# Kernel tuning notes

Measured on AMD Instinct MI355X. Metric: run time of the kernel, lower is better.

## Reference

```python
import jax, jax.numpy as jnp
import numpy as np

B, S, D = 2, 2048, 1024
H = 16
DK = D // H  # 64


def _rope_tables():
    # standard RoPE frequencies, shaped (1,1,S,DK//2) for clean broadcasting
    half = DK // 2
    inv_freq = 1.0 / (10000.0 ** (np.arange(0, half, dtype=np.float32) * 2.0 / DK))
    t = np.arange(S, dtype=np.float32)
    ang = np.einsum('s,d->sd', t, inv_freq)  # (S, half)
    sin = jnp.asarray(np.sin(ang))[None, None]  # (1,1,S,half)
    cos = jnp.asarray(np.cos(ang))[None, None]
    return sin, cos


def setup_inputs() -> dict:
    key = jax.random.key(0)
    ks = jax.random.split(key, 12)
    scale = 1.0 / np.sqrt(D)
    k = jax.random.normal(ks[0], (B, S, D), jnp.float32)
    q = jax.random.normal(ks[1], (B, S, D), jnp.float32)
    v = jax.random.normal(ks[2], (B, S, D), jnp.float32)
    # causal mask, broadcast over batch and heads: (1,1,S,S)
    mask = jnp.tril(jnp.ones((S, S), jnp.int32))[None, None]
    sin, cos = _rope_tables()
    Wk = jax.random.normal(ks[3], (D, D), jnp.float32) * scale
    bk = jax.random.normal(ks[4], (D,), jnp.float32) * scale
    Wq = jax.random.normal(ks[5], (D, D), jnp.float32) * scale
    bq = jax.random.normal(ks[6], (D,), jnp.float32) * scale
    Wv = jax.random.normal(ks[7], (D, D), jnp.float32) * scale
    bv = jax.random.normal(ks[8], (D,), jnp.float32) * scale
    Wo = jax.random.normal(ks[9], (D, D), jnp.float32) * scale
    bo = jax.random.normal(ks[10], (D,), jnp.float32) * scale
    return dict(k=k, q=q, v=v, mask=mask, sin=sin, cos=cos,
                Wk=Wk, bk=bk, Wq=Wq, bq=bq, Wv=Wv, bv=bv, Wo=Wo, bo=bo)


def _apply_rope(x, sin, cos):
    # x: (B,H,S,DK); sin/cos: (1,1,S,DK//2)
    x1 = x[..., ::2]
    x2 = x[..., 1::2]
    even = x1 * cos - x2 * sin
    odd = x1 * sin + x2 * cos
    return jnp.stack((even, odd), axis=-1).reshape(x.shape)


def reference(k, q, v, mask, sin, cos, Wk, bk, Wq, bq, Wv, bv, Wo, bo):
    # projections (nn.Linear: x @ W.T + b)
    def proj(x, W, b):
        y = x @ W.T + b
        return y.reshape(B, S, H, DK).transpose(0, 2, 1, 3)  # (B,H,S,DK)

    key = proj(k, Wk, bk)
    query = proj(q, Wq, bq)
    value = proj(v, Wv, bv)

    query = _apply_rope(query, sin, cos)
    key = _apply_rope(key, sin, cos)

    scores = jnp.einsum('bhqd,bhkd->bhqk', query, key) / jnp.sqrt(jnp.float32(DK))
    scores = jnp.where(mask == 0, jnp.float32(-1e9), scores)
    attn = jax.nn.softmax(scores, axis=-1)  # dropout=0 -> identity
    x = jnp.einsum('bhqk,bhkd->bhqd', attn, value)
    x = x.transpose(0, 2, 1, 3).reshape(B, S, D)
    return x @ Wo.T + bo
```

## Files before the change

kernel.cpp:

```cpp
#include <hip/hip_runtime.h>
#include <hip/hip_bf16.h>

typedef __bf16 bf16x8 __attribute__((ext_vector_type(8)));
typedef __bf16 bf16x4 __attribute__((ext_vector_type(4)));
typedef float  f32x4  __attribute__((ext_vector_type(4)));

static constexpr int B = 2, S = 2048, D = 1024, H = 16, DK = 64;
static constexpr int M = B * S;
static constexpr int NE = M * D;
static constexpr int WE = D * D;

__device__ inline float fast_exp2(float x) { return __builtin_amdgcn_exp2f(x); }

__device__ inline void gload16(const void* g, void* l) {
  __builtin_amdgcn_global_load_lds(
      (const __attribute__((address_space(1))) void*)g,
      (__attribute__((address_space(3))) void*)l, 16, 0, 0);
}

__device__ inline int perm64(int i) {
  return (((i >> 2) & 3) << 4) | (((i >> 5) & 1) << 3) | (((i >> 4) & 1) << 2) | (i & 3);
}

__global__ __launch_bounds__(256) void cvt_w(
    const float* __restrict__ Wq, const float* __restrict__ Wk,
    const float* __restrict__ Wv, const float* __restrict__ Wo,
    __bf16* __restrict__ Wall)
{
  int z = blockIdx.y;
  const float* src = (z == 0) ? Wq : (z == 1) ? Wk : (z == 2) ? Wv : Wo;
  __bf16* dst = Wall + (size_t)z * WE;
  int n4 = WE / 4;
  int i = blockIdx.x * blockDim.x + threadIdx.x;
  int stride = gridDim.x * blockDim.x;
  for (; i < n4; i += stride) {
    float4 f = reinterpret_cast<const float4*>(src)[i];
    bf16x4 o;
    o[0] = (__bf16)f.x; o[1] = (__bf16)f.y; o[2] = (__bf16)f.z; o[3] = (__bf16)f.w;
    reinterpret_cast<bf16x4*>(dst)[i] = o;
  }
}

__global__ __launch_bounds__(256, 4) void proj_kernel(
    const float* __restrict__ Xq32, const float* __restrict__ Xk32,
    const float* __restrict__ Xv32, const __bf16* __restrict__ Wall,
    const float* __restrict__ bq_, const float* __restrict__ bk_,
    const float* __restrict__ bv_,
    const float* __restrict__ sinp, const float* __restrict__ cosp,
    __bf16* __restrict__ Qr, __bf16* __restrict__ Kr, __bf16* __restrict__ Vt)
{
  __shared__ __align__(16) __bf16 Ws[128 * 64];
  __shared__ __align__(16) __bf16 Xs[128 * 64];
  int tid = threadIdx.x;
  int lane = tid & 63, wid = tid >> 6;
  int lr = lane & 15, lg = lane >> 4;
  int wr = wid >> 1, wc = wid & 1;
  int m0 = blockIdx.x * 128;
  int by = blockIdx.y;
  int z  = by >> 3;
  const float*  X32  = (z == 0) ? Xq32 : (z == 1) ? Xk32 : Xv32;
  const __bf16* Bw   = Wall + (size_t)by * 128 * 1024;
  const float*  bias = (z == 0) ? bq_ : (z == 1) ? bk_ : bv_;

  int wrow = tid >> 3;
  int wcol = 8 * ((tid & 7) ^ ((tid >> 3) & 7));
  char* wsbase = (char*)Ws + wid * 1024;

  int xrow = tid >> 3;
  int xcolf = (tid & 7) * 8;
  int xwb = ((tid & 7) * 16) ^ (((tid >> 3) & 7) << 4);

  f32x4 acc[4][4];
#pragma unroll
  for (int i = 0; i < 4; ++i)
#pragma unroll
    for (int j = 0; j < 4; ++j) acc[i][j] = (f32x4){0, 0, 0, 0};

  int fsw = (lr & 7) << 4;
  int foff0 = (lg * 16) ^ fsw;
  int foff1 = (64 + lg * 16) ^ fsw;

  bf16x8 xb[4];
#pragma unroll
  for (int p = 0; p < 4; ++p) {
    const float* xp = X32 + (size_t)(m0 + p * 32 + xrow) * 1024 + xcolf;
    f32x4 a = *(const f32x4*)(xp);
    f32x4 b = *(const f32x4*)(xp + 4);
    bf16x8 v;
#pragma unroll
    for (int e = 0; e < 4; ++e) { v[e] = (__bf16)a[e]; v[4 + e] = (__bf16)b[e]; }
    xb[p] = v;
  }

  for (int k0 = 0; k0 < 1024; k0 += 64) {
#pragma unroll
    for (int c = 0; c < 4; ++c)
      gload16(Bw + (size_t)(c * 32 + wrow) * 1024 + k0 + wcol,
              wsbase + c * 4096);
#pragma unroll
    for (int p = 0; p < 4; ++p)
      *(bf16x8*)((char*)Xs + (p * 32 + xrow) * 128 + xwb) = xb[p];
    __syncthreads();
    if (k0 + 64 < 1024) {
#pragma unroll
      for (int p = 0; p < 4; ++p) {
        const float* xp = X32 + (size_t)(m0 + p * 32 + xrow) * 1024 + k0 + 64 + xcolf;
        f32x4 a = *(const f32x4*)(xp);
        f32x4 b = *(const f32x4*)(xp + 4);
        bf16x8 v;
#pragma unroll
        for (int e = 0; e < 4; ++e) { v[e] = (__bf16)a[e]; v[4 + e] = (__bf16)b[e]; }
        xb[p] = v;
      }
    }
#pragma unroll
    for (int h = 0; h < 2; ++h) {
      int fo = h ? foff1 : foff0;
      bf16x8 af[4], bfr[4];
#pragma unroll
      for (int mi = 0; mi < 4; ++mi)
        af[mi] = *(const bf16x8*)((char*)Ws + (wr * 64 + mi * 16 + lr) * 128 + fo);
#pragma unroll
      for (int ni = 0; ni < 4; ++ni)
        bfr[ni] = *(const bf16x8*)((char*)Xs + (wc * 64 + ni * 16 + lr) * 128 + fo);
#pragma unroll
      for (int mi = 0; mi < 4; ++mi)
#pragma unroll
        for (int ni = 0; ni < 4; ++ni)
          acc[mi][ni] = __builtin_amdgcn_mfma_f32_16x16x32_bf16(af[mi], bfr[ni], acc[mi][ni], 0, 0, 0);
    }
    __syncthreads();
  }

#pragma unroll
  for (int mi = 0; mi < 4; ++mi) {
    int dkf0 = by * 128 + wr * 64 + mi * 16 + lg * 4;
    int col0 = dkf0 & 1023;
    int h = col0 >> 6, dk0 = col0 & 63, t0 = dk0 >> 1;
    float4 bv4 = *reinterpret_cast<const float4*>(&bias[col0]);
#pragma unroll
    for (int ni = 0; ni < 4; ++ni) {
      int r = m0 + wc * 64 + ni * 16 + lr;
      int s = r & (S - 1), bb = r >> 11;
      float v0 = acc[mi][ni][0] + bv4.x;
      float v1 = acc[mi][ni][1] + bv4.y;
      float v2 = acc[mi][ni][2] + bv4.z;
      float v3 = acc[mi][ni][3] + bv4.w;
      if (z < 2) {
        float2 sn = *reinterpret_cast<const float2*>(&sinp[s * 32 + t0]);
        float2 cs = *reinterpret_cast<const float2*>(&cosp[s * 32 + t0]);
        float e0 = v0 * cs.x - v1 * sn.x, o0 = v0 * sn.x + v1 * cs.x;
        float e1 = v2 * cs.y - v3 * sn.y, o1 = v2 * sn.y + v3 * cs.y;
        if (z == 0) {
          e0 *= 0.18033688011112042f; o0 *= 0.18033688011112042f;
          e1 *= 0.18033688011112042f; o1 *= 0.18033688011112042f;
        }
        bf16x4 w;
        w[0] = (__bf16)e0; w[1] = (__bf16)o0; w[2] = (__bf16)e1; w[3] = (__bf16)o1;
        __bf16* dst = (z == 0) ? Qr : Kr;
        *(bf16x4*)&dst[((size_t)(bb * H + h) * S + s) * DK + dk0] = w;
      } else {
        int sp = (s & ~63) | perm64(s & 63);
        size_t base = ((size_t)(bb * H + h) * DK + dk0) * S + sp;
        Vt[base]         = (__bf16)v0;
        Vt[base + S]     = (__bf16)v1;
        Vt[base + 2 * S] = (__bf16)v2;
        Vt[base + 3 * S] = (__bf16)v3;
      }
    }
  }
}

__global__ __launch_bounds__(256) void outproj_kernel(
    const __bf16* __restrict__ AO, const __bf16* __restrict__ Wo,
    const float* __restrict__ bo_, float* __restrict__ out)
{
  __shared__ __align__(16) __bf16 As[64 * 32];
  __shared__ __align__(16) __bf16 Bs[128 * 32];
  int tid = threadIdx.x;
  int lane = tid & 63, wid = tid >> 6;
  int lr = lane & 15, lg = lane >> 4;
  int wr = wid >> 1, wc = wid & 1;
  int m0 = blockIdx.x * 64;
  int n0 = blockIdx.y * 128;

  int arow = tid >> 2;
  int acol = (tid & 3) * 8;
  int brow = tid >> 2;
  int bcol = (tid & 3) * 8;
  char* asw = (char*)As + wid * 1024;
  char* bsw = (char*)Bs + wid * 1024;

  f32x4 acc[4][2];
#pragma unroll
  for (int i = 0; i < 4; ++i)
#pragma unroll
    for (int j = 0; j < 2; ++j) acc[i][j] = (f32x4){0, 0, 0, 0};

  for (int k0 = 0; k0 < 1024; k0 += 32) {
    gload16(AO + (size_t)(m0 + arow) * 1024 + k0 + acol, asw);
    gload16(Wo + (size_t)(n0 + brow) * 1024 + k0 + bcol, bsw);
    gload16(Wo + (size_t)(n0 + brow + 64) * 1024 + k0 + bcol, bsw + 4096);
    __syncthreads();
    bf16x8 wf[4], aof[2];
#pragma unroll
    for (int mi = 0; mi < 4; ++mi)
      wf[mi]  = *reinterpret_cast<const bf16x8*>(&Bs[(wr*64 + mi*16 + lr)*32 + lg*8]);
#pragma unroll
    for (int ni = 0; ni < 2; ++ni)
      aof[ni] = *reinterpret_cast<const bf16x8*>(&As[(wc*32 + ni*16 + lr)*32 + lg*8]);
#pragma unroll
    for (int mi = 0; mi < 4; ++mi)
#pragma unroll
      for (int ni = 0; ni < 2; ++ni)
        acc[mi][ni] = __builtin_amdgcn_mfma_f32_16x16x32_bf16(wf[mi], aof[ni], acc[mi][ni], 0, 0, 0);
    __syncthreads();
  }

#pragma unroll
  for (int mi = 0; mi < 4; ++mi) {
    int c0 = n0 + wr * 64 + mi * 16 + lg * 4;
    float4 bv4 = *reinterpret_cast<const float4*>(&bo_[c0]);
#pragma unroll
    for (int ni = 0; ni < 2; ++ni) {
      int r = m0 + wc * 32 + ni * 16 + lr;
      float4 w;
      w.x = acc[mi][ni][0] + bv4.x;
      w.y = acc[mi][ni][1] + bv4.y;
      w.z = acc[mi][ni][2] + bv4.z;
      w.w = acc[mi][ni][3] + bv4.w;
      *reinterpret_cast<float4*>(&out[(size_t)r * 1024 + c0]) = w;
    }
  }
}

__global__ __launch_bounds__(256, 4) void attn_kernel(
    const __bf16* __restrict__ Qr, const __bf16* __restrict__ Kr,
    const __bf16* __restrict__ Vt, __bf16* __restrict__ AO)
{
  __shared__ __align__(16) char smem[32768];
  int tid = threadIdx.x;
  int lane = tid & 63, wid = tid >> 6;
  int lr = lane & 15, lg = lane >> 4;
  int bx = blockIdx.x;
  int bh = (bx & 7) * 4 + ((bx >> 3) & 3);
  int qb = 31 - (bx >> 5);
  int q0 = qb * 64 + wid * 16;
  int nsteps = qb + 1;

  const char* Kb = (const char*)(Kr + (size_t)bh * S * DK);
  const char* Vb = (const char*)(Vt + (size_t)bh * DK * S);
  const __bf16* Qh = Qr + (size_t)bh * S * DK;

  int o_lo = wid * 1024 + lane * 16;
#define STAGE(sel, kv0)                                                        \
  {                                                                            \
    char* kdst = smem + (sel) * 16384;                                         \
    _Pragma("unroll")                                                          \
    for (int i = 0; i < 2; ++i) {                                              \
      int o = o_lo + i * 4096;                                                 \
      int row = o >> 7;                                                        \
      int colp = (o & 127) ^ ((row & 7) << 4);                                 \
      gload16(Kb + (((size_t)((kv0) + row)) << 7) + colp,                      \
              kdst + wid * 1024 + i * 4096);                                   \
      gload16(Vb + ((size_t)row * S + (kv0)) * 2 + colp,                       \
              kdst + 8192 + wid * 1024 + i * 4096);                            \
    }                                                                          \
  }

  bf16x8 bq[2];
#pragma unroll
  for (int kc = 0; kc < 2; ++kc)
    bq[kc] = *(const bf16x8*)(Qh + (size_t)(q0 + lr) * DK + kc * 32 + lg * 8);

  int swz = (lr & 7) << 4;
  int oK0 = lr * 128 + ((lg * 16) ^ swz);
  int oK1 = lr * 128 + ((64 + lg * 16) ^ swz);
  int oV0 = lr * 128 + ((lg * 32) ^ swz);
  int oV1 = lr * 128 + ((16 + lg * 32) ^ swz);

  f32x4 o[4];
  float m2 = -3e38f, l2 = 0.f;
#pragma unroll
  for (int dt = 0; dt < 4; ++dt) o[dt] = (f32x4){0, 0, 0, 0};

  STAGE(0, 0);
  __syncthreads();

  for (int j = 0; j < nsteps; ++j) {
    int sel = j & 1;
    if (j + 1 < nsteps) STAGE(sel ^ 1, (j + 1) * 64);
    const char* kbuf = smem + sel * 16384;
    const char* vbuf = kbuf + 8192;
    int kv0 = j * 64;

    f32x4 sc[4];
#pragma unroll
    for (int kt = 0; kt < 4; ++kt) {
      bf16x8 ka0 = *(const bf16x8*)(kbuf + oK0 + kt * 2048);
      bf16x8 ka1 = *(const bf16x8*)(kbuf + oK1 + kt * 2048);
      f32x4 s = (f32x4){0, 0, 0, 0};
      s = __builtin_amdgcn_mfma_f32_16x16x32_bf16(ka0, bq[0], s, 0, 0, 0);
      s = __builtin_amdgcn_mfma_f32_16x16x32_bf16(ka1, bq[1], s, 0, 0, 0);
      sc[kt] = s;
    }

    if (j == qb) {
#pragma unroll
      for (int kt = 0; kt < 4; ++kt)
#pragma unroll
        for (int i = 0; i < 4; ++i)
          if (kv0 + kt * 16 + lg * 4 + i > q0 + lr)
            sc[kt][i] = -3e38f;
    }

    float tm = fmaxf(
        fmaxf(fmaxf(fmaxf(sc[0][0], sc[0][1]), fmaxf(sc[0][2], sc[0][3])),
              fmaxf(fmaxf(sc[1][0], sc[1][1]), fmaxf(sc[1][2], sc[1][3]))),
        fmaxf(fmaxf(fmaxf(sc[2][0], sc[2][1]), fmaxf(sc[2][2], sc[2][3])),
              fmaxf(fmaxf(sc[3][0], sc[3][1]), fmaxf(sc[3][2], sc[3][3]))));
    tm = fmaxf(tm, __shfl_xor(tm, 16));
    tm = fmaxf(tm, __shfl_xor(tm, 32));
    if (__any(tm > m2 + 8.0f)) {
      float mn = fmaxf(m2, tm);
      float f = fast_exp2(m2 - mn);
      m2 = mn;
      l2 *= f;
#pragma unroll
      for (int dt = 0; dt < 4; ++dt) o[dt] *= f;
    }
    float p[16];
#pragma unroll
    for (int kt = 0; kt < 4; ++kt)
#pragma unroll
      for (int i = 0; i < 4; ++i)
        p[kt * 4 + i] = fast_exp2(sc[kt][i] - m2);
    float sum = (((p[0] + p[1]) + (p[2] + p[3])) + ((p[4] + p[5]) + (p[6] + p[7]))) +
                (((p[8] + p[9]) + (p[10] + p[11])) + ((p[12] + p[13]) + (p[14] + p[15])));
    sum += __shfl_xor(sum, 16);
    sum += __shfl_xor(sum, 32);
    l2 += sum;
    bf16x8 pb[2];
#pragma unroll
    for (int kc = 0; kc < 2; ++kc) {
      bf16x8 pv;
#pragma unroll
      for (int a = 0; a < 2; ++a)
#pragma unroll
        for (int r = 0; r < 4; ++r)
          pv[a * 4 + r] = (__bf16)p[(2 * kc + a) * 4 + r];
      pb[kc] = pv;
    }

#pragma unroll
    for (int dt = 0; dt < 4; ++dt) {
      bf16x8 v0 = *(const bf16x8*)(vbuf + oV0 + dt * 2048);
      bf16x8 v1 = *(const bf16x8*)(vbuf + oV1 + dt * 2048);
      o[dt] = __builtin_amdgcn_mfma_f32_16x16x32_bf16(v0, pb[0], o[dt], 0, 0, 0);
      o[dt] = __builtin_amdgcn_mfma_f32_16x16x32_bf16(v1, pb[1], o[dt], 0, 0, 0);
    }
    __syncthreads();
  }
#undef STAGE

  int b = bh >> 4, h = bh & 15;
  float inv = 1.f / l2;
  int s = q0 + lr;
#pragma unroll
  for (int dt = 0; dt < 4; ++dt) {
    bf16x4 w;
#pragma unroll
    for (int i = 0; i < 4; ++i) w[i] = (__bf16)(o[dt][i] * inv);
    *(bf16x4*)&AO[(((size_t)(b * S + s)) * H + h) * DK + dt * 16 + lg * 4] = w;
  }
}

extern "C" void kernel_launch(void* const* d_in, const int* in_sizes, int n_in,
                              void* d_out, int out_size, void* d_ws, size_t ws_size,
                              hipStream_t stream) {
  const float* k_in = (const float*)d_in[0];
  const float* q_in = (const float*)d_in[1];
  const float* v_in = (const float*)d_in[2];
  const float* sinp = (const float*)d_in[4];
  const float* cosp = (const float*)d_in[5];
  const float* Wk = (const float*)d_in[6];
  const float* bk = (const float*)d_in[7];
  const float* Wq = (const float*)d_in[8];
  const float* bq = (const float*)d_in[9];
  const float* Wv = (const float*)d_in[10];
  const float* bv = (const float*)d_in[11];
  const float* Wo = (const float*)d_in[12];
  const float* bo = (const float*)d_in[13];
  float* out = (float*)d_out;

  __bf16* ws   = (__bf16*)d_ws;
  __bf16* Wall = ws;
  __bf16* Qr   = ws + 4 * WE;
  __bf16* Kr   = Qr + NE;
  __bf16* Vt   = Kr + NE;
  __bf16* AO   = Vt + NE;

  dim3 blk(256);
  cvt_w<<<dim3(512, 4), blk, 0, stream>>>(Wq, Wk, Wv, Wo, Wall);
  proj_kernel<<<dim3(32, 24), blk, 0, stream>>>(q_in, k_in, v_in, Wall, bq, bk, bv,
                                                sinp, cosp, Qr, Kr, Vt);
  attn_kernel<<<1024, blk, 0, stream>>>(Qr, Kr, Vt, AO);
  outproj_kernel<<<dim3(64, 8), blk, 0, stream>>>(AO, Wall + 3 * WE, bo, out);
}
```

Before: 107.6 us.

## Double-buffer weight tiles in projection and out-projection GEMMs

Both GEMM kernels now keep two LDS buffers for the global-to-LDS weight (and activation) tiles and issue the next tile's async loads before the current tile's MFMAs. The goal is to overlap global load latency with compute and to cut one full __syncthreads per iteration. The projection kernel also holds raw fp32 X prefetches in registers and converts them just before the LDS store, and uses a bare s_barrier at the end of each iteration. The cost is double the LDS footprint and more live registers, which may lower occupancy. Correctness depends on the async LDS loads being complete before they are read, with only an s_barrier and no explicit vmcnt wait in between.

After: 127.7 us. 1.19x slower.

```diff
diff --git a/kernel.cpp b/kernel.cpp
--- a/kernel.cpp
+++ b/kernel.cpp
@@ -16,6 +16,12 @@
   __builtin_amdgcn_global_load_lds(
       (const __attribute__((address_space(1))) void*)g,
       (__attribute__((address_space(3))) void*)l, 16, 0, 0);
+}
+
+__device__ inline void bare_barrier() {
+  asm volatile("" ::: "memory");
+  __builtin_amdgcn_s_barrier();
+  asm volatile("" ::: "memory");
 }
 
 __device__ inline int perm64(int i) {
@@ -49,7 +55,7 @@
     const float* __restrict__ sinp, const float* __restrict__ cosp,
     __bf16* __restrict__ Qr, __bf16* __restrict__ Kr, __bf16* __restrict__ Vt)
 {
-  __shared__ __align__(16) __bf16 Ws[128 * 64];
+  __shared__ __align__(16) __bf16 Ws[2 * 128 * 64];
   __shared__ __align__(16) __bf16 Xs[128 * 64];
   int tid = threadIdx.x;
   int lane = tid & 63, wid = tid >> 6;
@@ -64,11 +70,10 @@
 
   int wrow = tid >> 3;
   int wcol = 8 * ((tid & 7) ^ ((tid >> 3) & 7));
-  char* wsbase = (char*)Ws + wid * 1024;
-
   int xrow = tid >> 3;
   int xcolf = (tid & 7) * 8;
   int xwb = ((tid & 7) * 16) ^ (((tid >> 3) & 7) << 4);
+  const float* xbase = X32 + (size_t)(m0 + xrow) * 1024 + xcolf;
 
   f32x4 acc[4][4];
 #pragma unroll
@@ -80,46 +85,52 @@
   int foff0 = (lg * 16) ^ fsw;
   int foff1 = (64 + lg * 16) ^ fsw;
 
-  bf16x8 xb[4];
+  f32x4 xf[8];
 #pragma unroll
   for (int p = 0; p < 4; ++p) {
-    const float* xp = X32 + (size_t)(m0 + p * 32 + xrow) * 1024 + xcolf;
-    f32x4 a = *(const f32x4*)(xp);
-    f32x4 b = *(const f32x4*)(xp + 4);
-    bf16x8 v;
-#pragma unroll
-    for (int e = 0; e < 4; ++e) { v[e] = (__bf16)a[e]; v[4 + e] = (__bf16)b[e]; }
-    xb[p] = v;
-  }
-
-  for (int k0 = 0; k0 < 1024; k0 += 64) {
+    xf[2*p]   = *(const f32x4*)(xbase + p * 32 * 1024);
+    xf[2*p+1] = *(const f32x4*)(xbase + p * 32 * 1024 + 4);
+  }
+  {
+    char* wd = (char*)Ws + wid * 1024;
 #pragma unroll
     for (int c = 0; c < 4; ++c)
-      gload16(Bw + (size_t)(c * 32 + wrow) * 1024 + k0 + wcol,
-              wsbase + c * 4096);
-#pragma unroll
-    for (int p = 0; p < 4; ++p)
-      *(bf16x8*)((char*)Xs + (p * 32 + xrow) * 128 + xwb) = xb[p];
+      gload16(Bw + (size_t)(c * 32 + wrow) * 1024 + wcol, wd + c * 4096);
+  }
+
+#pragma clang loop unroll(disable)
+  for (int t = 0; t < 16; ++t) {
+    int k0 = t * 64;
+    int kn = (t < 15) ? k0 + 64 : k0;
+#pragma unroll
+    for (int p = 0; p < 4; ++p) {
+      bf16x8 v;
+#pragma unroll
+      for (int e = 0; e < 4; ++e) {
+        v[e] = (__bf16)xf[2*p][e]; v[4+e] = (__bf16)xf[2*p+1][e];
+      }
+      *(bf16x8*)((char*)Xs + (p * 32 + xrow) * 128 + xwb) = v;
+    }
     __syncthreads();
-    if (k0 + 64 < 1024) {
-#pragma unroll
-      for (int p = 0; p < 4; ++p) {
-        const float* xp = X32 + (size_t)(m0 + p * 32 + xrow) * 1024 + k0 + 64 + xcolf;
-        f32x4 a = *(const f32x4*)(xp);
-        f32x4 b = *(const f32x4*)(xp + 4);
-        bf16x8 v;
-#pragma unroll
-        for (int e = 0; e < 4; ++e) { v[e] = (__bf16)a[e]; v[4 + e] = (__bf16)b[e]; }
-        xb[p] = v;
-      }
-    }
+#pragma unroll
+    for (int p = 0; p < 4; ++p) {
+      xf[2*p]   = *(const f32x4*)(xbase + p * 32 * 1024 + kn);
+      xf[2*p+1] = *(const f32x4*)(xbase + p * 32 * 1024 + kn + 4);
+    }
+    {
+      char* wd = (char*)Ws + (((t + 1) & 1) << 14) + wid * 1024;
+#pragma unroll
+      for (int c = 0; c < 4; ++c)
+        gload16(Bw + (size_t)(c * 32 + wrow) * 1024 + kn + wcol, wd + c * 4096);
+    }
+    const char* wsr = (const char*)Ws + ((t & 1) << 14);
 #pragma unroll
     for (int h = 0; h < 2; ++h) {
       int fo = h ? foff1 : foff0;
       bf16x8 af[4], bfr[4];
 #pragma unroll
       for (int mi = 0; mi < 4; ++mi)
-        af[mi] = *(const bf16x8*)((char*)Ws + (wr * 64 + mi * 16 + lr) * 128 + fo);
+        af[mi] = *(const bf16x8*)(wsr + (wr * 64 + mi * 16 + lr) * 128 + fo);
 #pragma unroll
       for (int ni = 0; ni < 4; ++ni)
         bfr[ni] = *(const bf16x8*)((char*)Xs + (wc * 64 + ni * 16 + lr) * 128 + fo);
@@ -129,7 +140,7 @@
         for (int ni = 0; ni < 4; ++ni)
           acc[mi][ni] = __builtin_amdgcn_mfma_f32_16x16x32_bf16(af[mi], bfr[ni], acc[mi][ni], 0, 0, 0);
     }
-    __syncthreads();
+    bare_barrier();
   }
 
 #pragma unroll
@@ -175,8 +186,8 @@
     const __bf16* __restrict__ AO, const __bf16* __restrict__ Wo,
     const float* __restrict__ bo_, float* __restrict__ out)
 {
-  __shared__ __align__(16) __bf16 As[64 * 32];
-  __shared__ __align__(16) __bf16 Bs[128 * 32];
+  __shared__ __align__(16) __bf16 As[2 * 64 * 32];
+  __shared__ __align__(16) __bf16 Bs[2 * 128 * 32];
   int tid = threadIdx.x;
   int lane = tid & 63, wid = tid >> 6;
   int lr = lane & 15, lg = lane >> 4;
@@ -186,10 +197,6 @@
 
   int arow = tid >> 2;
   int acol = (tid & 3) * 8;
-  int brow = tid >> 2;
-  int bcol = (tid & 3) * 8;
-  char* asw = (char*)As + wid * 1024;
-  char* bsw = (char*)Bs + wid * 1024;
 
   f32x4 acc[4][2];
 #pragma unroll
@@ -197,24 +204,39 @@
 #pragma unroll
     for (int j = 0; j < 2; ++j) acc[i][j] = (f32x4){0, 0, 0, 0};
 
-  for (int k0 = 0; k0 < 1024; k0 += 32) {
-    gload16(AO + (size_t)(m0 + arow) * 1024 + k0 + acol, asw);
-    gload16(Wo + (size_t)(n0 + brow) * 1024 + k0 + bcol, bsw);
-    gload16(Wo + (size_t)(n0 + brow + 64) * 1024 + k0 + bcol, bsw + 4096);
+  {
+    char* asw = (char*)As + wid * 1024;
+    char* bsw = (char*)Bs + wid * 1024;
+    gload16(AO + (size_t)(m0 + arow) * 1024 + acol, asw);
+    gload16(Wo + (size_t)(n0 + arow) * 1024 + acol, bsw);
+    gload16(Wo + (size_t)(n0 + arow + 64) * 1024 + acol, bsw + 4096);
+  }
+
+#pragma clang loop unroll(disable)
+  for (int t = 0; t < 32; ++t) {
+    int kn = (t < 31) ? (t + 1) * 32 : t * 32;
     __syncthreads();
+    {
+      char* asw = (char*)As + (((t + 1) & 1) << 12) + wid * 1024;
+      char* bsw = (char*)Bs + (((t + 1) & 1) << 13) + wid * 1024;
+      gload16(AO + (size_t)(m0 + arow) * 1024 + kn + acol, asw);
+      gload16(Wo + (size_t)(n0 + arow) * 1024 + kn + acol, bsw);
+      gload16(Wo + (size_t)(n0 + arow + 64) * 1024 + kn + acol, bsw + 4096);
+    }
+    const __bf16* as = (const __bf16*)((const char*)As + ((t & 1) << 12));
+    const __bf16* bs = (const __bf16*)((const char*)Bs + ((t & 1) << 13));
     bf16x8 wf[4], aof[2];
 #pragma unroll
     for (int mi = 0; mi < 4; ++mi)
-      wf[mi]  = *reinterpret_cast<const bf16x8*>(&Bs[(wr*64 + mi*16 + lr)*32 + lg*8]);
+      wf[mi]  = *reinterpret_cast<const bf16x8*>(&bs[(wr*64 + mi*16 + lr)*32 + lg*8]);
 #pragma unroll
     for (int ni = 0; ni < 2; ++ni)
-      aof[ni] = *reinterpret_cast<const bf16x8*>(&As[(wc*32 + ni*16 + lr)*32 + lg*8]);
+      aof[ni] = *reinterpret_cast<const bf16x8*>(&as[(wc*32 + ni*16 + lr)*32 + lg*8]);
 #pragma unroll
     for (int mi = 0; mi < 4; ++mi)
 #pragma unroll
       for (int ni = 0; ni < 2; ++ni)
         acc[mi][ni] = __builtin_amdgcn_mfma_f32_16x16x32_bf16(wf[mi], aof[ni], acc[mi][ni], 0, 0, 0);
-    __syncthreads();
   }
 
 #pragma unroll
```

## Coalesce projection epilogue stores via LDS staging and transposed V MFMA

Applied to the files above, without the earlier changes.

The Q/K epilogue now stages rotated bf16 results in shared memory with an XOR swizzle and writes them out as 16-byte row-contiguous stores instead of scattered 8-byte ones. For V, the MFMA operands are swapped so each lane holds four consecutive sequence positions, letting the transposed Vt be written with bf16x4 vector stores rather than four scalar strided stores. The X prefetch now keeps fp32 values in registers and converts at LDS-store time, which raises register pressure. This adds a barrier and extra LDS traffic in the epilogue.

Result: slower. 375.6 us (+249.0%).

```diff
diff --git a/kernel.cpp b/kernel.cpp
--- a/kernel.cpp
+++ b/kernel.cpp
@@ -49,8 +49,9 @@
     const float* __restrict__ sinp, const float* __restrict__ cosp,
     __bf16* __restrict__ Qr, __bf16* __restrict__ Kr, __bf16* __restrict__ Vt)
 {
-  __shared__ __align__(16) __bf16 Ws[128 * 64];
-  __shared__ __align__(16) __bf16 Xs[128 * 64];
+  __shared__ __align__(16) char psm[32768];
+  char* Wsc = psm;
+  char* Xsc = psm + 16384;
   int tid = threadIdx.x;
   int lane = tid & 63, wid = tid >> 6;
   int lr = lane & 15, lg = lane >> 4;
@@ -64,11 +65,12 @@
 
   int wrow = tid >> 3;
   int wcol = 8 * ((tid & 7) ^ ((tid >> 3) & 7));
-  char* wsbase = (char*)Ws + wid * 1024;
+  char* wsbase = Wsc + wid * 1024;
 
   int xrow = tid >> 3;
   int xcolf = (tid & 7) * 8;
   int xwb = ((tid & 7) * 16) ^ (((tid >> 3) & 7) << 4);
+  const float* xbase = X32 + (size_t)(m0 + xrow) * 1024 + xcolf;
 
   f32x4 acc[4][4];
 #pragma unroll
@@ -80,38 +82,44 @@
   int foff0 = (lg * 16) ^ fsw;
   int foff1 = (64 + lg * 16) ^ fsw;
 
-  bf16x8 xb[4];
-#pragma unroll
-  for (int p = 0; p < 4; ++p) {
-    const float* xp = X32 + (size_t)(m0 + p * 32 + xrow) * 1024 + xcolf;
-    f32x4 a = *(const f32x4*)(xp);
-    f32x4 b = *(const f32x4*)(xp + 4);
-    bf16x8 v;
-#pragma unroll
-    for (int e = 0; e < 4; ++e) { v[e] = (__bf16)a[e]; v[4 + e] = (__bf16)b[e]; }
-    xb[p] = v;
-  }
+  f32x4 xa0 = *(const f32x4*)(xbase);
+  f32x4 xa1 = *(const f32x4*)(xbase + 4);
+  f32x4 xa2 = *(const f32x4*)(xbase + 32 * 1024);
+  f32x4 xa3 = *(const f32x4*)(xbase + 32 * 1024 + 4);
+  f32x4 xa4 = *(const f32x4*)(xbase + 64 * 1024);
+  f32x4 xa5 = *(const f32x4*)(xbase + 64 * 1024 + 4);
+  f32x4 xa6 = *(const f32x4*)(xbase + 96 * 1024);
+  f32x4 xa7 = *(const f32x4*)(xbase + 96 * 1024 + 4);
 
   for (int k0 = 0; k0 < 1024; k0 += 64) {
 #pragma unroll
     for (int c = 0; c < 4; ++c)
-      gload16(Bw + (size_t)(c * 32 + wrow) * 1024 + k0 + wcol,
-              wsbase + c * 4096);
-#pragma unroll
-    for (int p = 0; p < 4; ++p)
-      *(bf16x8*)((char*)Xs + (p * 32 + xrow) * 128 + xwb) = xb[p];
+      gload16(Bw + (size_t)(c * 32 + wrow) * 1024 + k0 + wcol, wsbase + c * 4096);
+    {
+      bf16x8 v0, v1, v2, v3;
+#pragma unroll
+      for (int e = 0; e < 4; ++e) {
+        v0[e] = (__bf16)xa0[e]; v0[4+e] = (__bf16)xa1[e];
+        v1[e] = (__bf16)xa2[e]; v1[4+e] = (__bf16)xa3[e];
+        v2[e] = (__bf16)xa4[e]; v2[4+e] = (__bf16)xa5[e];
+        v3[e] = (__bf16)xa6[e]; v3[4+e] = (__bf16)xa7[e];
+      }
+      *(bf16x8*)(Xsc + (0 * 32 + xrow) * 128 + xwb) = v0;
+      *(bf16x8*)(Xsc + (1 * 32 + xrow) * 128 + xwb) = v1;
+      *(bf16x8*)(Xsc + (2 * 32 + xrow) * 128 + xwb) = v2;
+      *(bf16x8*)(Xsc + (3 * 32 + xrow) * 128 + xwb) = v3;
+    }
     __syncthreads();
     if (k0 + 64 < 1024) {
-#pragma unroll
-      for (int p = 0; p < 4; ++p) {
-        const float* xp = X32 + (size_t)(m0 + p * 32 + xrow) * 1024 + k0 + 64 + xcolf;
-        f32x4 a = *(const f32x4*)(xp);
-        f32x4 b = *(const f32x4*)(xp + 4);
-        bf16x8 v;
-#pragma unroll
-        for (int e = 0; e < 4; ++e) { v[e] = (__bf16)a[e]; v[4 + e] = (__bf16)b[e]; }
-        xb[p] = v;
-      }
+      const float* xn = xbase + k0 + 64;
+      xa0 = *(const f32x4*)(xn);
+      xa1 = *(const f32x4*)(xn + 4);
+      xa2 = *(const f32x4*)(xn + 32 * 1024);
+      xa3 = *(const f32x4*)(xn + 32 * 1024 + 4);
+      xa4 = *(const f32x4*)(xn + 64 * 1024);
+      xa5 = *(const f32x4*)(xn + 64 * 1024 + 4);
+      xa6 = *(const f32x4*)(xn + 96 * 1024);
+      xa7 = *(const f32x4*)(xn + 96 * 1024 + 4);
     }
 #pragma unroll
     for (int h = 0; h < 2; ++h) {
@@ -119,34 +127,43 @@
       bf16x8 af[4], bfr[4];
 #pragma unroll
       for (int mi = 0; mi < 4; ++mi)
-        af[mi] = *(const bf16x8*)((char*)Ws + (wr * 64 + mi * 16 + lr) * 128 + fo);
+        af[mi] = *(const bf16x8*)(Wsc + (wr * 64 + mi * 16 + lr) * 128 + fo);
 #pragma unroll
       for (int ni = 0; ni < 4; ++ni)
-        bfr[ni] = *(const bf16x8*)((char*)Xs + (wc * 64 + ni * 16 + lr) * 128 + fo);
-#pragma unroll
-      for (int mi = 0; mi < 4; ++mi)
-#pragma unroll
-        for (int ni = 0; ni < 4; ++ni)
-          acc[mi][ni] = __builtin_amdgcn_mfma_f32_16x16x32_bf16(af[mi], bfr[ni], acc[mi][ni], 0, 0, 0);
-    }
-    __syncthreads();
-  }
-
-#pragma unroll
-  for (int mi = 0; mi < 4; ++mi) {
-    int dkf0 = by * 128 + wr * 64 + mi * 16 + lg * 4;
-    int col0 = dkf0 & 1023;
-    int h = col0 >> 6, dk0 = col0 & 63, t0 = dk0 >> 1;
-    float4 bv4 = *reinterpret_cast<const float4*>(&bias[col0]);
-#pragma unroll
-    for (int ni = 0; ni < 4; ++ni) {
-      int r = m0 + wc * 64 + ni * 16 + lr;
-      int s = r & (S - 1), bb = r >> 11;
-      float v0 = acc[mi][ni][0] + bv4.x;
-      float v1 = acc[mi][ni][1] + bv4.y;
-      float v2 = acc[mi][ni][2] + bv4.z;
-      float v3 = acc[mi][ni][3] + bv4.w;
+        bfr[ni] = *(const bf16x8*)(Xsc + (wc * 64 + ni * 16 + lr) * 128 + fo);
       if (z < 2) {
+#pragma unroll
+        for (int mi = 0; mi < 4; ++mi)
+#pragma unroll
+          for (int ni = 0; ni < 4; ++ni)
+            acc[mi][ni] = __builtin_amdgcn_mfma_f32_16x16x32_bf16(af[mi], bfr[ni], acc[mi][ni], 0, 0, 0);
+      } else {
+#pragma unroll
+        for (int mi = 0; mi < 4; ++mi)
+#pragma unroll
+          for (int ni = 0; ni < 4; ++ni)
+            acc[mi][ni] = __builtin_amdgcn_mfma_f32_16x16x32_bf16(bfr[ni], af[mi], acc[mi][ni], 0, 0, 0);
+      }
+    }
+    __syncthreads();
+  }
+
+  if (z < 2) {
+    char* L = psm;
+#pragma unroll
+    for (int mi = 0; mi < 4; ++mi) {
+      int dkb = wr * 64 + mi * 16 + lg * 4;
+      int col0 = (by * 128 + dkb) & 1023;
+      int t0 = (col0 & 63) >> 1;
+      float4 bv4 = *reinterpret_cast<const float4*>(&bias[col0]);
+#pragma unroll
+      for (int ni = 0; ni < 4; ++ni) {
+        int srow = wc * 64 + ni * 16 + lr;
+        int s = (m0 + srow) & (S - 1);
+        float v0 = acc[mi][ni][0] + bv4.x;
+        float v1 = acc[mi][ni][1] + bv4.y;
+        float v2 = acc[mi][ni][2] + bv4.z;
+        float v3 = acc[mi][ni][3] + bv4.w;
         float2 sn = *reinterpret_cast<const float2*>(&sinp[s * 32 + t0]);
         float2 cs = *reinterpret_cast<const float2*>(&cosp[s * 32 + t0]);
         float e0 = v0 * cs.x - v1 * sn.x, o0 = v0 * sn.x + v1 * cs.x;
@@ -157,15 +174,37 @@
         }
         bf16x4 w;
         w[0] = (__bf16)e0; w[1] = (__bf16)o0; w[2] = (__bf16)e1; w[3] = (__bf16)o1;
-        __bf16* dst = (z == 0) ? Qr : Kr;
-        *(bf16x4*)&dst[((size_t)(bb * H + h) * S + s) * DK + dk0] = w;
-      } else {
-        int sp = (s & ~63) | perm64(s & 63);
-        size_t base = ((size_t)(bb * H + h) * DK + dk0) * S + sp;
-        Vt[base]         = (__bf16)v0;
-        Vt[base + S]     = (__bf16)v1;
-        Vt[base + 2 * S] = (__bf16)v2;
-        Vt[base + 3 * S] = (__bf16)v3;
+        *(bf16x4*)(L + srow * 256 + ((dkb * 2) ^ ((srow & 7) << 4))) = w;
+      }
+    }
+    __syncthreads();
+    __bf16* dst = (z == 0) ? Qr : Kr;
+#pragma unroll
+    for (int it = 0; it < 8; ++it) {
+      int srow = (tid >> 4) + 16 * it;
+      int c = tid & 15;
+      bf16x8 v = *(const bf16x8*)(psm + srow * 256 + ((c * 16) ^ ((srow & 7) << 4)));
+      int r = m0 + srow;
+      int s = r & (S - 1), bb = r >> 11;
+      int col0 = (by * 128 + c * 8) & 1023;
+      int h = col0 >> 6, dk0 = col0 & 63;
+      *(bf16x8*)&dst[((size_t)(bb * H + h) * S + s) * DK + dk0] = v;
+    }
+  } else {
+#pragma unroll
+    for (int mi = 0; mi < 4; ++mi) {
+      int col0 = (by * 128 + wr * 64 + mi * 16 + lr) & 1023;
+      int h = col0 >> 6, dk = col0 & 63;
+      float bval = bias[col0];
+#pragma unroll
+      for (int ni = 0; ni < 4; ++ni) {
+        int s0 = m0 + wc * 64 + ni * 16 + lg * 4;
+        int sg = s0 & (S - 1), bb = s0 >> 11;
+        int sp = (sg & ~63) | perm64(sg & 63);
+        bf16x4 w;
+#pragma unroll
+        for (int i = 0; i < 4; ++i) w[i] = (__bf16)(acc[mi][ni][i] + bval);
+        *(bf16x4*)&Vt[((size_t)(bb * H + h) * DK + dk) * S + sp] = w;
       }
     }
   }
@@ -186,8 +225,6 @@
 
   int arow = tid >> 2;
   int acol = (tid & 3) * 8;
-  int brow = tid >> 2;
-  int bcol = (tid & 3) * 8;
   char* asw = (char*)As + wid * 1024;
   char* bsw = (char*)Bs + wid * 1024;
 
@@ -199,8 +236,8 @@
 
   for (int k0 = 0; k0 < 1024; k0 += 32) {
     gload16(AO + (size_t)(m0 + arow) * 1024 + k0 + acol, asw);
-    gload16(Wo + (size_t)(n0 + brow) * 1024 + k0 + bcol, bsw);
-    gload16(Wo + (size_t)(n0 + brow + 64) * 1024 + k0 + bcol, bsw + 4096);
+    gload16(Wo + (size_t)(n0 + arow) * 1024 + k0 + acol, bsw);
+    gload16(Wo + (size_t)(n0 + arow + 64) * 1024 + k0 + acol, bsw + 4096);
     __syncthreads();
     bf16x8 wf[4], aof[2];
 #pragma unroll
```

## Double-buffer projection GEMM LDS tiles with K=32 steps and two-deep prefetch

Applied to the files above, without the earlier changes.

Restructures the QKV projection main loop to use two shared-memory buffers with a 32-wide K step. The next tile's weights (async global-to-LDS) and converted activations are written into the other buffer while MFMAs run on the current one, and fp32 activations are loaded two steps ahead. This removes the second barrier per iteration and is meant to hide load latency, at the cost of more iterations, doubled shared memory and a new swizzle scheme. The output projection change is only a variable rename.

New measurement: 114.9 us. 1.07x slower.

```diff
diff --git a/kernel.cpp b/kernel.cpp
--- a/kernel.cpp
+++ b/kernel.cpp
@@ -49,8 +49,7 @@
     const float* __restrict__ sinp, const float* __restrict__ cosp,
     __bf16* __restrict__ Qr, __bf16* __restrict__ Kr, __bf16* __restrict__ Vt)
 {
-  __shared__ __align__(16) __bf16 Ws[128 * 64];
-  __shared__ __align__(16) __bf16 Xs[128 * 64];
+  __shared__ __align__(16) char smem[32768];
   int tid = threadIdx.x;
   int lane = tid & 63, wid = tid >> 6;
   int lr = lane & 15, lg = lane >> 4;
@@ -62,13 +61,16 @@
   const __bf16* Bw   = Wall + (size_t)by * 128 * 1024;
   const float*  bias = (z == 0) ? bq_ : (z == 1) ? bk_ : bv_;
 
-  int wrow = tid >> 3;
-  int wcol = 8 * ((tid & 7) ^ ((tid >> 3) & 7));
-  char* wsbase = (char*)Ws + wid * 1024;
-
-  int xrow = tid >> 3;
-  int xcolf = (tid & 7) * 8;
-  int xwb = ((tid & 7) * 16) ^ (((tid >> 3) & 7) << 4);
+  int wrb   = wid * 16 + (lane >> 2);
+  int wcolE = ((lane & 3) * 8) ^ (((lane >> 2) & 3) << 3);
+
+  int xr = tid >> 1, xc = tid & 1;
+  const float* xbase = X32 + (size_t)(m0 + xr) * 1024 + xc * 16;
+  int xswz = (xr & 3) << 4;
+  int xo0 = xr * 64 + ((xc * 32) ^ xswz);
+  int xo1 = xr * 64 + ((xc * 32 + 16) ^ xswz);
+
+  int foff = (lg * 16) ^ ((lr & 3) << 4);
 
   f32x4 acc[4][4];
 #pragma unroll
@@ -76,53 +78,62 @@
 #pragma unroll
     for (int j = 0; j < 4; ++j) acc[i][j] = (f32x4){0, 0, 0, 0};
 
-  int fsw = (lr & 7) << 4;
-  int foff0 = (lg * 16) ^ fsw;
-  int foff1 = (64 + lg * 16) ^ fsw;
-
-  bf16x8 xb[4];
-#pragma unroll
-  for (int p = 0; p < 4; ++p) {
-    const float* xp = X32 + (size_t)(m0 + p * 32 + xrow) * 1024 + xcolf;
-    f32x4 a = *(const f32x4*)(xp);
-    f32x4 b = *(const f32x4*)(xp + 4);
-    bf16x8 v;
-#pragma unroll
-    for (int e = 0; e < 4; ++e) { v[e] = (__bf16)a[e]; v[4 + e] = (__bf16)b[e]; }
-    xb[p] = v;
-  }
-
-  for (int k0 = 0; k0 < 1024; k0 += 64) {
-#pragma unroll
-    for (int c = 0; c < 4; ++c)
-      gload16(Bw + (size_t)(c * 32 + wrow) * 1024 + k0 + wcol,
-              wsbase + c * 4096);
-#pragma unroll
-    for (int p = 0; p < 4; ++p)
-      *(bf16x8*)((char*)Xs + (p * 32 + xrow) * 128 + xwb) = xb[p];
-    __syncthreads();
-    if (k0 + 64 < 1024) {
-#pragma unroll
-      for (int p = 0; p < 4; ++p) {
-        const float* xp = X32 + (size_t)(m0 + p * 32 + xrow) * 1024 + k0 + 64 + xcolf;
-        f32x4 a = *(const f32x4*)(xp);
-        f32x4 b = *(const f32x4*)(xp + 4);
-        bf16x8 v;
-#pragma unroll
-        for (int e = 0; e < 4; ++e) { v[e] = (__bf16)a[e]; v[4 + e] = (__bf16)b[e]; }
-        xb[p] = v;
+  f32x4 xa0 = *(const f32x4*)(xbase);
+  f32x4 xa1 = *(const f32x4*)(xbase + 4);
+  f32x4 xa2 = *(const f32x4*)(xbase + 8);
+  f32x4 xa3 = *(const f32x4*)(xbase + 12);
+  {
+    bf16x8 lo, hi;
+#pragma unroll
+    for (int e = 0; e < 4; ++e) {
+      lo[e] = (__bf16)xa0[e]; lo[4 + e] = (__bf16)xa1[e];
+      hi[e] = (__bf16)xa2[e]; hi[4 + e] = (__bf16)xa3[e];
+    }
+    *(bf16x8*)(smem + 8192 + xo0) = lo;
+    *(bf16x8*)(smem + 8192 + xo1) = hi;
+    char* wd = smem + wid * 1024;
+    gload16(Bw + (size_t)wrb * 1024 + wcolE, wd);
+    gload16(Bw + (size_t)(64 + wrb) * 1024 + wcolE, wd + 4096);
+  }
+  xa0 = *(const f32x4*)(xbase + 32);
+  xa1 = *(const f32x4*)(xbase + 36);
+  xa2 = *(const f32x4*)(xbase + 40);
+  xa3 = *(const f32x4*)(xbase + 44);
+  __syncthreads();
+
+#pragma clang loop unroll(disable)
+  for (int t = 0; t < 32; ++t) {
+    int cur = t & 1, nxt = cur ^ 1;
+    char* bufC = smem + cur * 16384;
+    char* bufN = smem + nxt * 16384;
+    int kn  = (t < 31) ? (t + 1) * 32 : 31 * 32;
+    int kn2 = (t < 30) ? (t + 2) * 32 : 31 * 32;
+
+    {
+      char* wd = bufN + wid * 1024;
+      gload16(Bw + (size_t)wrb * 1024 + kn + wcolE, wd);
+      gload16(Bw + (size_t)(64 + wrb) * 1024 + kn + wcolE, wd + 4096);
+      bf16x8 lo, hi;
+#pragma unroll
+      for (int e = 0; e < 4; ++e) {
+        lo[e] = (__bf16)xa0[e]; lo[4 + e] = (__bf16)xa1[e];
+        hi[e] = (__bf16)xa2[e]; hi[4 + e] = (__bf16)xa3[e];
       }
-    }
-#pragma unroll
-    for (int h = 0; h < 2; ++h) {
-      int fo = h ? foff1 : foff0;
+      *(bf16x8*)(bufN + 8192 + xo0) = lo;
+      *(bf16x8*)(bufN + 8192 + xo1) = hi;
+    }
+    xa0 = *(const f32x4*)(xbase + kn2);
+    xa1 = *(const f32x4*)(xbase + kn2 + 4);
+    xa2 = *(const f32x4*)(xbase + kn2 + 8);
+    xa3 = *(const f32x4*)(xbase + kn2 + 12);
+    {
       bf16x8 af[4], bfr[4];
 #pragma unroll
       for (int mi = 0; mi < 4; ++mi)
-        af[mi] = *(const bf16x8*)((char*)Ws + (wr * 64 + mi * 16 + lr) * 128 + fo);
+        af[mi] = *(const bf16x8*)(bufC + (wr * 64 + mi * 16 + lr) * 64 + foff);
 #pragma unroll
       for (int ni = 0; ni < 4; ++ni)
-        bfr[ni] = *(const bf16x8*)((char*)Xs + (wc * 64 + ni * 16 + lr) * 128 + fo);
+        bfr[ni] = *(const bf16x8*)(bufC + 8192 + (wc * 64 + ni * 16 + lr) * 64 + foff);
 #pragma unroll
       for (int mi = 0; mi < 4; ++mi)
 #pragma unroll
@@ -186,8 +197,6 @@
 
   int arow = tid >> 2;
   int acol = (tid & 3) * 8;
-  int brow = tid >> 2;
-  int bcol = (tid & 3) * 8;
   char* asw = (char*)As + wid * 1024;
   char* bsw = (char*)Bs + wid * 1024;
 
@@ -199,8 +208,8 @@
 
   for (int k0 = 0; k0 < 1024; k0 += 32) {
     gload16(AO + (size_t)(m0 + arow) * 1024 + k0 + acol, asw);
-    gload16(Wo + (size_t)(n0 + brow) * 1024 + k0 + bcol, bsw);
-    gload16(Wo + (size_t)(n0 + brow + 64) * 1024 + k0 + bcol, bsw + 4096);
+    gload16(Wo + (size_t)(n0 + arow) * 1024 + k0 + acol, bsw);
+    gload16(Wo + (size_t)(n0 + arow + 64) * 1024 + k0 + acol, bsw + 4096);
     __syncthreads();
     bf16x8 wf[4], aof[2];
 #pragma unroll
```
